# Kernel optimization log

Measured on AMD Instinct MI355X. Metric: run time of the kernel, lower is better.

The kernel has to match this reference:

```python
import jax, jax.numpy as jnp
import numpy as np

N_EMBD = 768
N_HEAD = 12
DIM_HEAD = N_EMBD // N_HEAD


def setup_inputs() -> dict:
    key = jax.random.key(0)
    k1, k2, k3 = jax.random.split(key, 3)
    B, T = 4, 2048
    x = jax.random.normal(k1, (B, T, N_EMBD), dtype=jnp.float32)
    # torch Linear(n_embd, 3*n_embd, bias=False): y = x @ W.T, W:[3C,C].
    # Store pre-transposed [C,3C] for direct matmul.
    s = 1.0 / np.sqrt(N_EMBD)
    W_qkv = jax.random.uniform(k2, (N_EMBD, 3 * N_EMBD), dtype=jnp.float32, minval=-s, maxval=s)
    W_proj = jax.random.uniform(k3, (N_EMBD, N_EMBD), dtype=jnp.float32, minval=-s, maxval=s)
    return {"x": x, "W_qkv": W_qkv, "W_proj": W_proj}


def reference(x, W_qkv, W_proj):
    B, T, C = x.shape
    qkv = x @ W_qkv                                  # [B,T,3C]
    q, k, v = jnp.split(qkv, 3, axis=-1)
    def heads(t):  # [B,T,C] -> [B,H,T,Dh]
        return t.reshape(B, T, N_HEAD, DIM_HEAD).transpose(0, 2, 1, 3)
    q, k, v = heads(q), heads(k), heads(v)
    # Source divides by scale = dim_head**-0.5, i.e. multiplies by sqrt(dim_head).
    scores = jnp.einsum('bhtd,bhsd->bhts', q, k) * jnp.sqrt(jnp.float32(DIM_HEAD))
    attn = jax.nn.softmax(scores, axis=-1)           # [B,H,T,T] materialized
    y = jnp.einsum('bhts,bhsd->bhtd', attn, v)       # [B,H,T,Dh]
    y = y.transpose(0, 2, 1, 3).reshape(B, T, C)
    return y @ W_proj
```

## Files before the change

kernel.cpp:

```cpp
#include <hip/hip_runtime.h>

typedef _Float16 f16;
typedef f16 f16x4 __attribute__((ext_vector_type(4)));
typedef f16 f16x8 __attribute__((ext_vector_type(8)));
typedef __fp16 h16x2 __attribute__((ext_vector_type(2)));
typedef float floatx4 __attribute__((ext_vector_type(4)));

#define LDT 72
#define LDE 136
#define QSCALE 11.5415603271117f

__device__ __forceinline__ void gld16(const void* g, void* l) {
  __builtin_amdgcn_global_load_lds((const __attribute__((address_space(1))) unsigned int*)g,
                                   (__attribute__((address_space(3))) unsigned int*)l,
                                   16, 0, 0);
}

__device__ __forceinline__ void transpose_tile(const float* __restrict__ in,
                                               f16* __restrict__ out,
                                               int K, int N, int bx, int by) {
  __shared__ f16 tile[64][LDT];
  int k0 = bx * 64, n0 = by * 64;
  int tid = threadIdx.x;
  int r = tid >> 4, c4 = (tid & 15) * 4;
  for (int p = 0; p < 4; ++p) {
    int rr = r + p * 16;
    float4 v = *(const float4*)(in + (size_t)(k0 + rr) * N + n0 + c4);
    tile[c4 + 0][rr] = (f16)v.x;
    tile[c4 + 1][rr] = (f16)v.y;
    tile[c4 + 2][rr] = (f16)v.z;
    tile[c4 + 3][rr] = (f16)v.w;
  }
  __syncthreads();
  int rn = tid >> 3, ck = (tid & 7) * 8;
  for (int p = 0; p < 2; ++p) {
    int rr = rn + p * 32;
    *(uint4*)(out + (size_t)(n0 + rr) * K + k0 + ck) = *(const uint4*)(&tile[rr][ck]);
  }
}

__global__ __launch_bounds__(256) void prep(const float* __restrict__ x,
                                            f16* __restrict__ x16,
                                            const float* __restrict__ Wqkv,
                                            f16* __restrict__ WqkvT,
                                            const float* __restrict__ Wproj,
                                            f16* __restrict__ WprojT) {
  int bid = blockIdx.x;
  if (bid < 3072) {
    size_t i = ((size_t)bid * 256 + threadIdx.x) * 8;
    float4 v0 = *(const float4*)(x + i);
    float4 v1 = *(const float4*)(x + i + 4);
    f16x8 h = {(f16)v0.x, (f16)v0.y, (f16)v0.z, (f16)v0.w,
               (f16)v1.x, (f16)v1.y, (f16)v1.z, (f16)v1.w};
    *(f16x8*)(x16 + i) = h;
  } else if (bid < 3504) {
    int t = bid - 3072;
    transpose_tile(Wqkv, WqkvT, 768, 2304, t % 12, t / 12);
  } else {
    int t = bid - 3504;
    transpose_tile(Wproj, WprojT, 768, 768, t % 12, t / 12);
  }
}


#define GEMM_DEFS                                                        \
  int tid = threadIdx.x;                                                 \
  int lane = tid & 63, wid = tid >> 6;                                   \
  int quad = lane >> 4, l16 = lane & 15;                                 \
  int wy = wid >> 1, wx = wid & 1;                                       \
  int m0 = blockIdx.x * 128, n0 = blockIdx.y * 128;                      \
  int gr = lane >> 3;                                                    \
  int gcs = ((lane & 7) ^ gr) * 8;

#define STG(AOFF, BOFF, K0)                                              \
  do {                                                                   \
    _Pragma("unroll") for (int p = 0; p < 4; ++p) {                      \
      gld16(aSrc + (size_t)p * 8 * strA + (K0), smem + (AOFF) + (wid * 4 + p) * 512); \
      gld16(bSrc + (size_t)p * 8 * strB + (K0), smem + (BOFF) + (wid * 4 + p) * 512); \
    }                                                                    \
  } while (0)

#define CMP(AOFF, BOFF)                                                  \
  do {                                                                   \
    _Pragma("unroll") for (int kk8 = 0; kk8 < 8; kk8 += 4) {             \
      f16x8 af[4], bfr[4];                                               \
      _Pragma("unroll") for (int i = 0; i < 4; ++i)                      \
        af[i] = *(const f16x8*)(smem + (AOFF) + (wy * 64 + i * 16 + l16) * 64 + \
                                (((kk8 + quad) ^ (l16 & 7)) * 8));       \
      _Pragma("unroll") for (int j = 0; j < 4; ++j)                      \
        bfr[j] = *(const f16x8*)(smem + (BOFF) + (wx * 64 + j * 16 + l16) * 64 + \
                                 (((kk8 + quad) ^ (l16 & 7)) * 8));      \
      _Pragma("unroll") for (int i = 0; i < 4; ++i)                      \
        _Pragma("unroll") for (int j = 0; j < 4; ++j)                    \
          acc[i][j] = __builtin_amdgcn_mfma_f32_16x16x32_f16(af[i], bfr[j], acc[i][j], 0, 0, 0); \
    }                                                                    \
  } while (0)

__global__ __launch_bounds__(256) void gemm1_qkv(const f16* __restrict__ A,
                                                 const f16* __restrict__ Bt,
                                                 f16* __restrict__ q16, f16* __restrict__ k16,
                                                 f16* __restrict__ vt) {
  __shared__ f16 smem[32768];
  GEMM_DEFS
  const int strA = 768, strB = 768;
  const f16* aSrc = A + (size_t)(m0 + wid * 32 + gr) * 768 + gcs;
  const f16* bSrc = Bt + (size_t)(n0 + wid * 32 + gr) * 768 + gcs;
  floatx4 acc[4][4] = {};

  STG(0, 8192, 0);
  __syncthreads();
#pragma unroll 1
  for (int k2 = 0; k2 < 6; ++k2) {
    STG(16384, 24576, (2 * k2 + 1) * 64);
    CMP(0, 8192);
    __syncthreads();
    if (k2 < 5) STG(0, 8192, (2 * k2 + 2) * 64);
    CMP(16384, 24576);
    __syncthreads();
  }

  int b = m0 >> 11, t0 = m0 & 2047;
  if (n0 < 1536) {
    for (int i = 0; i < 4; ++i)
      for (int j = 0; j < 4; ++j)
        for (int r = 0; r < 4; ++r) {
          int t = t0 + wy * 64 + i * 16 + quad * 4 + r;
          int col = n0 + wx * 64 + j * 16 + l16;
          float a = acc[i][j][r];
          if (col < 768) {
            int h = col >> 6, d = col & 63;
            q16[((size_t)(b * 12 + h)) * 131072 + (size_t)t * 64 + d] = (f16)(a * QSCALE);
          } else {
            int c = col - 768;
            int h = c >> 6, d = c & 63;
            k16[((size_t)(b * 12 + h)) * 131072 + (size_t)t * 64 + d] = (f16)a;
          }
        }
  } else {
    f16* Vtile = smem;
    int h0 = (n0 - 1536) >> 6;
    for (int i = 0; i < 4; ++i)
      for (int j = 0; j < 4; ++j) {
        int cl = wx * 64 + j * 16 + l16;
        int rl = wy * 64 + i * 16 + quad * 4;
        for (int r = 0; r < 4; ++r)
          Vtile[cl * LDE + rl + r] = (f16)acc[i][j][r];
      }
    __syncthreads();
    int u = tid & 15;
    for (int p = 0; p < 8; ++p) {
      int c = (tid >> 4) + p * 16;
      *(uint4*)(vt + ((size_t)(b * 12 + h0 + (c >> 6))) * 131072 +
                (size_t)(c & 63) * 2048 + t0 + u * 8) =
          *(const uint4*)(Vtile + c * LDE + u * 8);
    }
  }
}

__global__ __launch_bounds__(256) void gemm_bt_f16(const f16* __restrict__ A,
                                                   const f16* __restrict__ Bt,
                                                   float* __restrict__ C,
                                                   int M, int N, int K) {
  __shared__ f16 smem[32768];
  GEMM_DEFS
  const int strA = K, strB = K;
  const f16* aSrc = A + (size_t)(m0 + wid * 32 + gr) * K + gcs;
  const f16* bSrc = Bt + (size_t)(n0 + wid * 32 + gr) * K + gcs;
  floatx4 acc[4][4] = {};
  int nk2 = K >> 7;

  STG(0, 8192, 0);
  __syncthreads();
#pragma unroll 1
  for (int k2 = 0; k2 < nk2; ++k2) {
    STG(16384, 24576, (2 * k2 + 1) * 64);
    CMP(0, 8192);
    __syncthreads();
    if (k2 < nk2 - 1) STG(0, 8192, (2 * k2 + 2) * 64);
    CMP(16384, 24576);
    __syncthreads();
  }

  for (int i = 0; i < 4; ++i) {
    int row = m0 + wy * 64 + i * 16 + quad * 4;
    for (int j = 0; j < 4; ++j) {
      int col = n0 + wx * 64 + j * 16 + l16;
      for (int r = 0; r < 4; ++r)
        C[(size_t)(row + r) * N + col] = acc[i][j][r];
    }
  }
}

__global__ __launch_bounds__(512, 1) void flash_attn(const f16* __restrict__ q16,
                                                     const f16* __restrict__ k16,
                                                     const f16* __restrict__ vT,
                                                     f16* __restrict__ y) {
  __shared__ f16 Ks[128 * 64];
  __shared__ f16 Vt[64 * 128];
  const int T = 2048;
  int xcd = blockIdx.x & 7, yb = blockIdx.x >> 3;
  int bh = xcd * 6 + (yb >> 4);
  int qt = yb & 15;
  int b = bh / 12, h = bh - b * 12;
  int tid = threadIdx.x;
  int lane = tid & 63, wid = tid >> 6;
  int quad = lane >> 4, l16 = lane & 15;
  int rk = tid >> 3, kch = tid & 7;
  int rv = tid >> 4, vch = tid & 15;
  int kswz = (kch ^ (rk & 7)) * 8;
  int vswz = (vch ^ (rv & 15)) * 8;
  size_t hb = (size_t)bh * T * 64;

  f16x8 qf[2];
  {
    size_t qrow = hb + (size_t)(qt * 128 + wid * 16 + l16) * 64 + quad * 8;
    qf[0] = *(const f16x8*)(q16 + qrow);
    qf[1] = *(const f16x8*)(q16 + qrow + 32);
  }
  f16x8 ones8;
  for (int e = 0; e < 8; ++e) ones8[e] = (f16)1.0f;

  float m_i = -1e30f, l_i = 0.f;
  floatx4 o[4] = {};

  for (int kt = 0; kt < 16; ++kt) {
    if (kt) __syncthreads();
    for (int p = 0; p < 2; ++p) {
      int r = rk + p * 64;
      *(uint4*)(Ks + r * 64 + kswz) =
          *(const uint4*)(k16 + hb + (size_t)(kt * 128 + r) * 64 + kch * 8);
      int d = rv + p * 32;
      *(uint4*)(Vt + d * 128 + vswz) =
          *(const uint4*)(vT + hb + (size_t)d * T + kt * 128 + vch * 8);
    }
    __syncthreads();

    floatx4 sf[8];
    const floatx4 z4 = {0.f, 0.f, 0.f, 0.f};
    for (int i = 0; i < 8; ++i) sf[i] = z4;
    for (int kk = 0; kk < 2; ++kk)
      for (int i = 0; i < 8; ++i) {
        int row = i * 16 + l16;
        f16x8 kf = *(const f16x8*)(Ks + row * 64 + (((kk * 4 + quad) ^ (l16 & 7)) * 8));
        sf[i] = __builtin_amdgcn_mfma_f32_16x16x32_f16(kf, qf[kk], sf[i], 0, 0, 0);
      }

    float mx = fmaxf(fmaxf(sf[0][0], sf[0][1]), fmaxf(sf[0][2], sf[0][3]));
    for (int i = 1; i < 8; ++i)
      mx = fmaxf(mx, fmaxf(fmaxf(sf[i][0], sf[i][1]), fmaxf(sf[i][2], sf[i][3])));
    mx = fmaxf(mx, __shfl_xor(mx, 16));
    mx = fmaxf(mx, __shfl_xor(mx, 32));
    float m_new = fmaxf(m_i, mx);
    float alpha = exp2f(m_i - m_new);
    m_i = m_new;
    for (int i = 0; i < 4; ++i) o[i] *= alpha;

    f16x4 pf[8];
    for (int i = 0; i < 8; ++i) {
      union { h16x2 h; f16 f[2]; } a2, b2;
      a2.h = __builtin_amdgcn_cvt_pkrtz(sf[i][0] - m_new, sf[i][1] - m_new);
      b2.h = __builtin_amdgcn_cvt_pkrtz(sf[i][2] - m_new, sf[i][3] - m_new);
      f16x4 uu = {a2.f[0], a2.f[1], b2.f[0], b2.f[1]};
#if __has_builtin(__builtin_elementwise_exp2)
      pf[i] = __builtin_elementwise_exp2(uu);
#else
      for (int r = 0; r < 4; ++r) pf[i][r] = (f16)exp2f((float)uu[r]);
#endif
    }

    floatx4 rs = z4;
    for (int i = 0; i < 4; ++i) {
      f16x8 pp = {pf[2 * i][0], pf[2 * i][1], pf[2 * i][2], pf[2 * i][3],
                  pf[2 * i + 1][0], pf[2 * i + 1][1], pf[2 * i + 1][2], pf[2 * i + 1][3]};
      rs = __builtin_amdgcn_mfma_f32_16x16x32_f16(ones8, pp, rs, 0, 0, 0);
    }
    l_i = l_i * alpha + rs[0];

    for (int i = 0; i < 4; ++i)
      for (int si = 0; si < 8; ++si) {
        int d = i * 16 + l16;
        int cch = si * 2 + (quad >> 1);
        f16x4 vf = *(const f16x4*)(Vt + d * 128 + ((cch ^ l16) * 8) + (quad & 1) * 4);
        o[i] = __builtin_amdgcn_mfma_f32_16x16x16f16(vf, pf[si], o[i], 0, 0, 0);
      }
  }

  float invl = 1.0f / l_i;
  int t = qt * 128 + wid * 16 + l16;
  size_t off = ((size_t)(b * T + t)) * 768 + h * 64;
  for (int i = 0; i < 4; ++i)
    for (int r = 0; r < 4; ++r)
      y[off + i * 16 + quad * 4 + r] = (f16)(o[i][r] * invl);
}

extern "C" void kernel_launch(void* const* d_in, const int* in_sizes, int n_in,
                              void* d_out, int out_size, void* d_ws, size_t ws_size,
                              hipStream_t stream) {
  const float* x     = (const float*)d_in[0];
  const float* Wqkv  = (const float*)d_in[1];
  const float* Wproj = (const float*)d_in[2];
  float* out = (float*)d_out;
  char* ws = (char*)d_ws;
  f16* q16    = (f16*)ws;
  f16* k16    = (f16*)(ws + 12582912);
  f16* vT16   = (f16*)(ws + 25165824);
  f16* y16    = (f16*)(ws + 37748736);
  f16* WqkvT  = (f16*)(ws + 50331648);
  f16* WprojT = (f16*)(ws + 53870592);
  f16* x16 = y16;

  prep<<<3648, 256, 0, stream>>>(x, x16, Wqkv, WqkvT, Wproj, WprojT);
  gemm1_qkv<<<dim3(64, 18), 256, 0, stream>>>(x16, WqkvT, q16, k16, vT16);
  flash_attn<<<768, 512, 0, stream>>>(q16, k16, vT16, y16);
  gemm_bt_f16<<<dim3(64, 6), 256, 0, stream>>>(y16, WprojT, out, 8192, 768, 768);
}
```

Baseline: 224.1 us.

## Drop double-buffered staging in GEMMs and use 16x16x16 MFMA for row sums

Both GEMM kernels move from a two-stage double-buffered LDS pipeline to a single-buffer loop: load a 64-wide K slice, synchronise, compute, repeat. This halves shared memory per block, which may allow more blocks per CU, but global loads no longer overlap with MFMA work. In the attention kernel the row-sum reduction now uses eight 16x16x16 MFMAs on the existing P fragments instead of four 16x16x32 MFMAs on repacked pairs, removing the register shuffles but issuing more instructions.

```diff
diff --git a/kernel.cpp b/kernel.cpp
--- a/kernel.cpp
+++ b/kernel.cpp
@@ -100,23 +100,19 @@
                                                  const f16* __restrict__ Bt,
                                                  f16* __restrict__ q16, f16* __restrict__ k16,
                                                  f16* __restrict__ vt) {
-  __shared__ f16 smem[32768];
+  __shared__ f16 smem[17408];
   GEMM_DEFS
   const int strA = 768, strB = 768;
   const f16* aSrc = A + (size_t)(m0 + wid * 32 + gr) * 768 + gcs;
   const f16* bSrc = Bt + (size_t)(n0 + wid * 32 + gr) * 768 + gcs;
   floatx4 acc[4][4] = {};
 
-  STG(0, 8192, 0);
-  __syncthreads();
 #pragma unroll 1
-  for (int k2 = 0; k2 < 6; ++k2) {
-    STG(16384, 24576, (2 * k2 + 1) * 64);
+  for (int k0 = 0; k0 < 12; ++k0) {
+    if (k0) __syncthreads();
+    STG(0, 8192, k0 * 64);
+    __syncthreads();
     CMP(0, 8192);
-    __syncthreads();
-    if (k2 < 5) STG(0, 8192, (2 * k2 + 2) * 64);
-    CMP(16384, 24576);
-    __syncthreads();
   }
 
   int b = m0 >> 11, t0 = m0 & 2047;
@@ -137,6 +133,7 @@
           }
         }
   } else {
+    __syncthreads();
     f16* Vtile = smem;
     int h0 = (n0 - 1536) >> 6;
     for (int i = 0; i < 4; ++i)
@@ -161,24 +158,20 @@
                                                    const f16* __restrict__ Bt,
                                                    float* __restrict__ C,
                                                    int M, int N, int K) {
-  __shared__ f16 smem[32768];
+  __shared__ f16 smem[16384];
   GEMM_DEFS
   const int strA = K, strB = K;
   const f16* aSrc = A + (size_t)(m0 + wid * 32 + gr) * K + gcs;
   const f16* bSrc = Bt + (size_t)(n0 + wid * 32 + gr) * K + gcs;
   floatx4 acc[4][4] = {};
-  int nk2 = K >> 7;
-
-  STG(0, 8192, 0);
-  __syncthreads();
+  int nk = K >> 6;
+
 #pragma unroll 1
-  for (int k2 = 0; k2 < nk2; ++k2) {
-    STG(16384, 24576, (2 * k2 + 1) * 64);
+  for (int k0 = 0; k0 < nk; ++k0) {
+    if (k0) __syncthreads();
+    STG(0, 8192, k0 * 64);
+    __syncthreads();
     CMP(0, 8192);
-    __syncthreads();
-    if (k2 < nk2 - 1) STG(0, 8192, (2 * k2 + 2) * 64);
-    CMP(16384, 24576);
-    __syncthreads();
   }
 
   for (int i = 0; i < 4; ++i) {
@@ -217,8 +210,8 @@
     qf[0] = *(const f16x8*)(q16 + qrow);
     qf[1] = *(const f16x8*)(q16 + qrow + 32);
   }
-  f16x8 ones8;
-  for (int e = 0; e < 8; ++e) ones8[e] = (f16)1.0f;
+  f16x4 ones4;
+  for (int e = 0; e < 4; ++e) ones4[e] = (f16)1.0f;
 
   float m_i = -1e30f, l_i = 0.f;
   floatx4 o[4] = {};
@@ -269,11 +262,8 @@
     }
 
     floatx4 rs = z4;
-    for (int i = 0; i < 4; ++i) {
-      f16x8 pp = {pf[2 * i][0], pf[2 * i][1], pf[2 * i][2], pf[2 * i][3],
-                  pf[2 * i + 1][0], pf[2 * i + 1][1], pf[2 * i + 1][2], pf[2 * i + 1][3]};
-      rs = __builtin_amdgcn_mfma_f32_16x16x32_f16(ones8, pp, rs, 0, 0, 0);
-    }
+    for (int si = 0; si < 8; ++si)
+      rs = __builtin_amdgcn_mfma_f32_16x16x16f16(ones4, pf[si], rs, 0, 0, 0);
     l_i = l_i * alpha + rs[0];
 
     for (int i = 0; i < 4; ++i)
```

Result: slower. 234.1 us (+4.5%).
